# Optimization experiments

Measured on AMD Instinct MI355X. Metric: run time of the kernel, lower is better.

Reference implementation:

```python
import jax, jax.numpy as jnp
import numpy as np

H = 256
V = 10000
E = 300000


def setup_inputs() -> dict:
    key = jax.random.key(0)
    ks = jax.random.split(key, 7)
    s = 1.0 / np.sqrt(H)  # torch nn.Linear default init scale
    x = jax.random.normal(ks[0], (V, H), dtype=jnp.float32)
    e = jax.random.normal(ks[1], (E, H), dtype=jnp.float32)
    edge_index = jax.random.randint(ks[2], (2, E), 0, V, dtype=jnp.int64)
    Us_w = jax.random.uniform(ks[3], (H, H), dtype=jnp.float32, minval=-s, maxval=s)
    Us_b = jax.random.uniform(ks[4], (H,), dtype=jnp.float32, minval=-s, maxval=s)
    Vs_w = jax.random.uniform(ks[5], (H, H), dtype=jnp.float32, minval=-s, maxval=s)
    Vs_b = jax.random.uniform(ks[6], (H,), dtype=jnp.float32, minval=-s, maxval=s)
    return {"x": x, "e": e, "edge_index": edge_index,
            "Us_w": Us_w, "Us_b": Us_b, "Vs_w": Vs_w, "Vs_b": Vs_b}


def reference(x, e, edge_index, Us_w, Us_b, Vs_w, Vs_b):
    # Ue = Us(e): (E, H); Vx = Vs(x): (V, H)  [torch Linear: y = x @ W.T + b]
    Ue = jnp.einsum('eh,oh->eo', e, Us_w) + Us_b
    Vx = jnp.einsum('vh,oh->vo', x, Vs_w) + Vs_b
    src, dst = edge_index[0], edge_index[1]
    # gather + add epilogue: e_new = Ue + Vx[src] + Vx[dst]
    e_new = Ue + Vx[src] + Vx[dst]
    return e_new
```

## Files before the change

kernel.cpp:

```cpp
#include <hip/hip_runtime.h>


typedef __bf16 bf16_t;
typedef __bf16 bf16x4 __attribute__((ext_vector_type(4)));
typedef __bf16 bf16x8 __attribute__((ext_vector_type(8)));
typedef float f32x4 __attribute__((ext_vector_type(4)));
typedef float f32x8 __attribute__((ext_vector_type(8)));

#define HDIM 256
#define NV 10000
#define NE 300000

__device__ __forceinline__ void async16(const bf16_t* g, bf16_t* l) {
  __builtin_amdgcn_global_load_lds(
      (const __attribute__((address_space(1))) void*)g,
      (__attribute__((address_space(3))) void*)l, 16, 0, 0);
}

__global__ __launch_bounds__(256) void cvt_weights(
    const float* __restrict__ us, const float* __restrict__ vs,
    bf16_t* __restrict__ us_o, bf16_t* __restrict__ vs_o) {
  const int c = blockIdx.x * 256 + threadIdx.x;
  const int h = c >> 12;
  const int idx = c & 4095;
  const int g2 = idx >> 6;
  const int ln = idx & 63;
  const int ni = g2 & 7;
  const int ks = g2 >> 3;
  const int n = h * 128 + ni * 16 + (ln & 15);
  const int kb = ks * 32 + (ln >> 4) * 8;
  const float* su = us + n * HDIM + kb;
  const float* sv = vs + n * HDIM + kb;
  f32x4 a0 = *(const f32x4*)su, a1 = *(const f32x4*)(su + 4);
  f32x4 b0 = *(const f32x4*)sv, b1 = *(const f32x4*)(sv + 4);
  f32x8 av = {a0[0], a0[1], a0[2], a0[3], a1[0], a1[1], a1[2], a1[3]};
  f32x8 bv = {b0[0], b0[1], b0[2], b0[3], b1[0], b1[1], b1[2], b1[3]};
  *(bf16x8*)(us_o + c * 8) = __builtin_convertvector(av, bf16x8);
  *(bf16x8*)(vs_o + c * 8) = __builtin_convertvector(bv, bf16x8);
}

template <bool FUSED>
__global__ __launch_bounds__(256, 2) void gemm(
    const float* __restrict__ A,
    const bf16_t* __restrict__ Wb,
    const float* __restrict__ bias,
    const int* __restrict__ sIdxG,
    const int* __restrict__ dIdxG,
    const bf16_t* __restrict__ Vx,
    float* __restrict__ outF,
    bf16_t* __restrict__ outB,
    int M) {
  __shared__ __align__(16) char smem[65536];

  const int tid = threadIdx.x;
  const int lane = tid & 63;
  const int wave = tid >> 6;
  const int l15 = lane & 15;
  const int quad = lane >> 4;

  const int n0 = blockIdx.x * 128;
  const int row0 = blockIdx.y * 128;

  const bf16_t* wsHalf = Wb + (size_t)blockIdx.x * 32768;
  bf16_t* lB = (bf16_t*)smem;
#pragma unroll
  for (int i = 0; i < 16; ++i) {
    const int c = tid + i * 256;
    async16(wsHalf + c * 8, lB + c * 8);
  }

  const float* pA[2];
#pragma unroll
  for (int mi = 0; mi < 2; ++mi) {
    int r = row0 + wave * 32 + mi * 16 + l15;
    if (r >= M) r = M - 1;
    pA[mi] = A + (size_t)r * HDIM + quad * 8;
  }
  f32x4 ar[8][2][2];
#pragma unroll
  for (int ks = 0; ks < 8; ++ks)
#pragma unroll
    for (int mi = 0; mi < 2; ++mi) {
      ar[ks][mi][0] = *(const f32x4*)(pA[mi] + ks * 32);
      ar[ks][mi][1] = *(const f32x4*)(pA[mi] + ks * 32 + 4);
    }

  f32x4 acc[2][8];
#pragma unroll
  for (int mi = 0; mi < 2; ++mi)
#pragma unroll
    for (int ni = 0; ni < 8; ++ni) {
      f32x4 z = {0.f, 0.f, 0.f, 0.f};
      acc[mi][ni] = z;
    }

  __syncthreads();

#pragma unroll
  for (int ks = 0; ks < 8; ++ks) {
    bf16x8 af[2];
#pragma unroll
    for (int mi = 0; mi < 2; ++mi) {
      f32x8 v = {ar[ks][mi][0][0], ar[ks][mi][0][1], ar[ks][mi][0][2],
                 ar[ks][mi][0][3], ar[ks][mi][1][0], ar[ks][mi][1][1],
                 ar[ks][mi][1][2], ar[ks][mi][1][3]};
      af[mi] = __builtin_convertvector(v, bf16x8);
    }
#pragma unroll
    for (int ni = 0; ni < 8; ++ni) {
      bf16x8 bfr = *(const bf16x8*)(smem + (ks * 8 + ni) * 1024 + lane * 16);
#pragma unroll
      for (int mi = 0; mi < 2; ++mi)
        acc[mi][ni] = __builtin_amdgcn_mfma_f32_16x16x32_bf16(
            af[mi], bfr, acc[mi][ni], 0, 0, 0);
    }
  }

  __syncthreads();

  float bcol[8];
#pragma unroll
  for (int ni = 0; ni < 8; ++ni)
    bcol[ni] = bias[n0 + ni * 16 + l15];

  float* stage = (float*)smem + wave * (16 * 132);
  const int srow = lane >> 2;
  const int scol = (lane & 3) * 4;

#pragma unroll
  for (int mi = 0; mi < 2; ++mi) {
#pragma unroll
    for (int ni = 0; ni < 8; ++ni)
#pragma unroll
      for (int r = 0; r < 4; ++r)
        stage[(quad * 4 + r) * 132 + ni * 16 + l15] = acc[mi][ni][r] + bcol[ni];

    const int row = row0 + wave * 32 + mi * 16 + srow;
    if (row < M) {
      const float* sp = stage + srow * 132;
      if constexpr (FUSED) {
        const int si = sIdxG[row];
        const int di = dIdxG[row];
        const bf16_t* vs = Vx + (size_t)si * HDIM + n0;
        const bf16_t* vd = Vx + (size_t)di * HDIM + n0;
        float* op = outF + (size_t)row * HDIM + n0;
#pragma unroll
        for (int i = 0; i < 8; ++i) {
          const int c = i * 16 + scol;
          f32x4 a = *(const f32x4*)(sp + c);
          f32x4 sf = __builtin_convertvector(*(const bf16x4*)(vs + c), f32x4);
          f32x4 df = __builtin_convertvector(*(const bf16x4*)(vd + c), f32x4);
          *(f32x4*)(op + c) = a + sf + df;
        }
      } else {
        bf16_t* op = outB + (size_t)row * HDIM + n0;
#pragma unroll
        for (int i = 0; i < 8; ++i) {
          const int c = i * 16 + scol;
          f32x4 a = *(const f32x4*)(sp + c);
          *(bf16x4*)(op + c) = __builtin_convertvector(a, bf16x4);
        }
      }
    }
  }
}

extern "C" void kernel_launch(void* const* d_in, const int* in_sizes, int n_in,
                              void* d_out, int out_size, void* d_ws,
                              size_t ws_size, hipStream_t stream) {
  const float* x = (const float*)d_in[0];
  const float* e = (const float*)d_in[1];
  const int* edge = (const int*)d_in[2];
  const float* Us_w = (const float*)d_in[3];
  const float* Us_b = (const float*)d_in[4];
  const float* Vs_w = (const float*)d_in[5];
  const float* Vs_b = (const float*)d_in[6];
  float* out = (float*)d_out;

  bf16_t* us_w_b = (bf16_t*)d_ws;
  bf16_t* vs_w_b = (bf16_t*)((char*)d_ws + (128 << 10));
  bf16_t* Vx = (bf16_t*)((char*)d_ws + (256 << 10));

  dim3 blk(256, 1, 1);

  cvt_weights<<<dim3(32, 1, 1), blk, 0, stream>>>(Us_w, Vs_w, us_w_b, vs_w_b);

  dim3 g1(2, (NV + 127) / 128, 1);
  gemm<false><<<g1, blk, 0, stream>>>(x, vs_w_b, Vs_b, nullptr, nullptr,
                                      nullptr, nullptr, Vx, NV);

  dim3 g2(2, (NE + 127) / 128, 1);
  gemm<true><<<g2, blk, 0, stream>>>(e, us_w_b, Us_b, edge, edge + NE, Vx, out,
                                     nullptr, NE);
}
```

Measured before the change: 563.5 us.

## Shrink GEMM N-tile to 64 with XCD-aware block remap and higher occupancy

Splits the output columns into four 64-wide tiles instead of two 128-wide ones. LDS drops to 32KB and the launch bound rises to 4 blocks per SU, aiming to raise occupancy and latency hiding in this memory-bound GEMM-plus-gather. A 1D grid with an XCD-aware remap puts the four column tiles of one row block on the same XCD so they share the fp32 A reads in L2. The trade-off is that each A row is now read and converted by four blocks instead of two, which adds MFMA-side conversion and load traffic.

After: 704.0 us. 1.25x slower.

```diff
diff --git a/kernel.cpp b/kernel.cpp
--- a/kernel.cpp
+++ b/kernel.cpp
@@ -21,13 +21,13 @@
     const float* __restrict__ us, const float* __restrict__ vs,
     bf16_t* __restrict__ us_o, bf16_t* __restrict__ vs_o) {
   const int c = blockIdx.x * 256 + threadIdx.x;
-  const int h = c >> 12;
-  const int idx = c & 4095;
+  const int h = c >> 11;
+  const int idx = c & 2047;
   const int g2 = idx >> 6;
   const int ln = idx & 63;
-  const int ni = g2 & 7;
-  const int ks = g2 >> 3;
-  const int n = h * 128 + ni * 16 + (ln & 15);
+  const int ni = g2 & 3;
+  const int ks = g2 >> 2;
+  const int n = h * 64 + ni * 16 + (ln & 15);
   const int kb = ks * 32 + (ln >> 4) * 8;
   const float* su = us + n * HDIM + kb;
   const float* sv = vs + n * HDIM + kb;
@@ -40,7 +40,7 @@
 }
 
 template <bool FUSED>
-__global__ __launch_bounds__(256, 2) void gemm(
+__global__ __launch_bounds__(256, 4) void gemm(
     const float* __restrict__ A,
     const bf16_t* __restrict__ Wb,
     const float* __restrict__ bias,
@@ -50,7 +50,7 @@
     float* __restrict__ outF,
     bf16_t* __restrict__ outB,
     int M) {
-  __shared__ __align__(16) char smem[65536];
+  __shared__ __align__(16) char smem[32768];
 
   const int tid = threadIdx.x;
   const int lane = tid & 63;
@@ -58,23 +58,28 @@
   const int l15 = lane & 15;
   const int quad = lane >> 4;
 
-  const int n0 = blockIdx.x * 128;
-  const int row0 = blockIdx.y * 128;
-
-  const bf16_t* wsHalf = Wb + (size_t)blockIdx.x * 32768;
+  const int Nb = gridDim.x;
+  const int q = Nb >> 3, r = Nb & 7;
+  const int xcd = blockIdx.x & 7, bidx = blockIdx.x >> 3;
+  const int lin = (xcd < r) ? (xcd * (q + 1) + bidx)
+                            : (r * (q + 1) + (xcd - r) * q + bidx);
+  const int n0 = (lin & 3) * 64;
+  const int row0 = (lin >> 2) * 128;
+
+  const bf16_t* wsQ = Wb + (size_t)(lin & 3) * 16384;
   bf16_t* lB = (bf16_t*)smem;
 #pragma unroll
-  for (int i = 0; i < 16; ++i) {
+  for (int i = 0; i < 8; ++i) {
     const int c = tid + i * 256;
-    async16(wsHalf + c * 8, lB + c * 8);
+    async16(wsQ + c * 8, lB + c * 8);
   }
 
   const float* pA[2];
 #pragma unroll
   for (int mi = 0; mi < 2; ++mi) {
-    int r = row0 + wave * 32 + mi * 16 + l15;
-    if (r >= M) r = M - 1;
-    pA[mi] = A + (size_t)r * HDIM + quad * 8;
+    int rr = row0 + wave * 32 + mi * 16 + l15;
+    if (rr >= M) rr = M - 1;
+    pA[mi] = A + (size_t)rr * HDIM + quad * 8;
   }
   f32x4 ar[8][2][2];
 #pragma unroll
@@ -85,11 +90,11 @@
       ar[ks][mi][1] = *(const f32x4*)(pA[mi] + ks * 32 + 4);
     }
 
-  f32x4 acc[2][8];
+  f32x4 acc[2][4];
 #pragma unroll
   for (int mi = 0; mi < 2; ++mi)
 #pragma unroll
-    for (int ni = 0; ni < 8; ++ni) {
+    for (int ni = 0; ni < 4; ++ni) {
       f32x4 z = {0.f, 0.f, 0.f, 0.f};
       acc[mi][ni] = z;
     }
@@ -107,8 +112,8 @@
       af[mi] = __builtin_convertvector(v, bf16x8);
     }
 #pragma unroll
-    for (int ni = 0; ni < 8; ++ni) {
-      bf16x8 bfr = *(const bf16x8*)(smem + (ks * 8 + ni) * 1024 + lane * 16);
+    for (int ni = 0; ni < 4; ++ni) {
+      bf16x8 bfr = *(const bf16x8*)(smem + (ks * 4 + ni) * 1024 + lane * 16);
 #pragma unroll
       for (int mi = 0; mi < 2; ++mi)
         acc[mi][ni] = __builtin_amdgcn_mfma_f32_16x16x32_bf16(
@@ -118,26 +123,27 @@
 
   __syncthreads();
 
-  float bcol[8];
-#pragma unroll
-  for (int ni = 0; ni < 8; ++ni)
+  float bcol[4];
+#pragma unroll
+  for (int ni = 0; ni < 4; ++ni)
     bcol[ni] = bias[n0 + ni * 16 + l15];
 
-  float* stage = (float*)smem + wave * (16 * 132);
+  float* stage = (float*)smem + wave * (16 * 68);
   const int srow = lane >> 2;
   const int scol = (lane & 3) * 4;
 
 #pragma unroll
   for (int mi = 0; mi < 2; ++mi) {
 #pragma unroll
-    for (int ni = 0; ni < 8; ++ni)
-#pragma unroll
-      for (int r = 0; r < 4; ++r)
-        stage[(quad * 4 + r) * 132 + ni * 16 + l15] = acc[mi][ni][r] + bcol[ni];
+    for (int ni = 0; ni < 4; ++ni)
+#pragma unroll
+      for (int rg = 0; rg < 4; ++rg)
+        stage[(quad * 4 + rg) * 68 + ni * 16 + l15] =
+            acc[mi][ni][rg] + bcol[ni];
 
     const int row = row0 + wave * 32 + mi * 16 + srow;
     if (row < M) {
-      const float* sp = stage + srow * 132;
+      const float* sp = stage + srow * 68;
       if constexpr (FUSED) {
         const int si = sIdxG[row];
         const int di = dIdxG[row];
@@ -145,7 +151,7 @@
         const bf16_t* vd = Vx + (size_t)di * HDIM + n0;
         float* op = outF + (size_t)row * HDIM + n0;
 #pragma unroll
-        for (int i = 0; i < 8; ++i) {
+        for (int i = 0; i < 4; ++i) {
           const int c = i * 16 + scol;
           f32x4 a = *(const f32x4*)(sp + c);
           f32x4 sf = __builtin_convertvector(*(const bf16x4*)(vs + c), f32x4);
@@ -155,7 +161,7 @@
       } else {
         bf16_t* op = outB + (size_t)row * HDIM + n0;
 #pragma unroll
-        for (int i = 0; i < 8; ++i) {
+        for (int i = 0; i < 4; ++i) {
           const int c = i * 16 + scol;
           f32x4 a = *(const f32x4*)(sp + c);
           *(bf16x4*)(op + c) = __builtin_convertvector(a, bf16x4);
@@ -185,11 +191,11 @@
 
   cvt_weights<<<dim3(32, 1, 1), blk, 0, stream>>>(Us_w, Vs_w, us_w_b, vs_w_b);
 
-  dim3 g1(2, (NV + 127) / 128, 1);
-  gemm<false><<<g1, blk, 0, stream>>>(x, vs_w_b, Vs_b, nullptr, nullptr,
-                                      nullptr, nullptr, Vx, NV);
-
-  dim3 g2(2, (NE + 127) / 128, 1);
-  gemm<true><<<g2, blk, 0, stream>>>(e, us_w_b, Us_b, edge, edge + NE, Vx, out,
-                                     nullptr, NE);
-}
+  const int n1 = 4 * ((NV + 127) / 128);
+  gemm<false><<<dim3(n1, 1, 1), blk, 0, stream>>>(
+      x, vs_w_b, Vs_b, nullptr, nullptr, nullptr, nullptr, Vx, NV);
+
+  const int n2 = 4 * ((NE + 127) / 128);
+  gemm<true><<<dim3(n2, 1, 1), blk, 0, stream>>>(
+      e, us_w_b, Us_b, edge, edge + NE, Vx, out, nullptr, NE);
+}
```
